# Optimization experiments

Measured on AMD Instinct MI355X. Metric: run time of the kernel, lower is better.

## Reference

```python
import jax, jax.numpy as jnp
import numpy as np

N_NODES = 50000


def setup_inputs() -> dict:
    key = jax.random.key(0)
    ks = jax.random.split(key, 5)
    d_in, d_out = 512, 512
    n_edges = 800000
    x = jax.random.normal(ks[0], (N_NODES, d_in), dtype=jnp.float32)
    edge_index = jax.random.randint(ks[1], (2, n_edges), 0, N_NODES, dtype=jnp.int64)
    s = 1.0 / np.sqrt(d_in)
    W_l = jax.random.uniform(ks[2], (d_out, d_in), dtype=jnp.float32, minval=-s, maxval=s)
    b_l = jax.random.uniform(ks[3], (d_out,), dtype=jnp.float32, minval=-s, maxval=s)
    W_r = jax.random.uniform(ks[4], (d_out, d_in), dtype=jnp.float32, minval=-s, maxval=s)
    return {"x": x, "edge_index": edge_index, "W_l": W_l, "b_l": b_l, "W_r": W_r}


def reference(x, edge_index, W_l, b_l, W_r):
    # lin_l: dense transform before aggregation
    x_l = x @ W_l.T + b_l                       # [N, d_out]
    src, dst = edge_index[0], edge_index[1]
    # sparse adjacency matmul (SAGE mean-neighbor aggregation):
    # out_l[i] = mean_{j in N(i)} x_l[j]
    agg = jax.ops.segment_sum(x_l[src], dst, num_segments=N_NODES)   # [N, d_out]
    deg = jax.ops.segment_sum(jnp.ones_like(src, dtype=x.dtype), dst,
                              num_segments=N_NODES)                  # [N]
    out_l = agg / jnp.maximum(deg, 1.0)[:, None]
    # lin_r: self-loop transform (no bias)
    out_r = x @ W_r.T
    return out_l + out_r
```

## Files before the change

kernel.cpp:

```cpp
#include <hip/hip_runtime.h>

typedef __bf16 bf16x8 __attribute__((ext_vector_type(8)));
typedef float floatx4 __attribute__((ext_vector_type(4)));
typedef float floatx2 __attribute__((ext_vector_type(2)));
typedef unsigned short ushortx8 __attribute__((ext_vector_type(8)));

__device__ __forceinline__ unsigned short f2b(float f) {
    union { float f; unsigned u; } v; v.f = f;
    unsigned r = v.u + 0x7fffu + ((v.u >> 16) & 1u);
    return (unsigned short)(r >> 16);
}


__global__ void scan_kernel(const int* __restrict__ deg, int* __restrict__ off,
                            int n, int nE) {
    __shared__ int s[256];
    __shared__ int base_s;
    int b = blockIdx.x, t = threadIdx.x;
    int lim = b * 1024;
    int acc = 0;
    for (int i = t * 4; i < lim; i += 1024) {
        int4 v = *(const int4*)(deg + i);
        acc += v.x + v.y + v.z + v.w;
    }
    s[t] = acc; __syncthreads();
    for (int o = 128; o > 0; o >>= 1) { if (t < o) s[t] += s[t + o]; __syncthreads(); }
    if (t == 0) base_s = s[0];
    __syncthreads();
    int idx = b * 1024 + t * 4;
    int a0 = (idx     < n) ? deg[idx]     : 0;
    int a1 = (idx + 1 < n) ? deg[idx + 1] : 0;
    int a2 = (idx + 2 < n) ? deg[idx + 2] : 0;
    int a3 = (idx + 3 < n) ? deg[idx + 3] : 0;
    int tsum = a0 + a1 + a2 + a3;
    s[t] = tsum; __syncthreads();
    for (int o = 1; o < 256; o <<= 1) {
        int u = (t >= o) ? s[t - o] : 0;
        __syncthreads();
        s[t] += u;
        __syncthreads();
    }
    int excl = s[t] - tsum + base_s;
    if (idx     < n) off[idx]     = excl;
    if (idx + 1 < n) off[idx + 1] = excl + a0;
    if (idx + 2 < n) off[idx + 2] = excl + a0 + a1;
    if (idx + 3 < n) off[idx + 3] = excl + a0 + a1 + a2;
    if (b == 0 && t == 0) off[n] = nE;
}

__global__ void fill_kernel(const int* __restrict__ src, const int* __restrict__ dst,
                            const int* __restrict__ off, int* __restrict__ cursor,
                            int* __restrict__ csr, int nE) {
    int e = blockIdx.x * blockDim.x + threadIdx.x;
    if (e < nE) {
        int d = dst[e];
        int pos = atomicAdd(&cursor[d], 1);
        csr[off[d] + pos] = src[e];
    }
}


__global__ void conv_kernel(const float* __restrict__ x, unsigned short* __restrict__ Abuf,
                            unsigned char* __restrict__ X8,
                            const float* __restrict__ Wl, const float* __restrict__ Wr,
                            unsigned short* __restrict__ Wcat,
                            const int* __restrict__ dst, int* __restrict__ deg, int nE,
                            int Mreal, long nx) {
    long t = (long)blockIdx.x * blockDim.x + threadIdx.x;
    if (t < nx) {
        long row = t >> 6;
        int c8 = (int)(t & 63) * 8;
        if (row < Mreal) {
            const float4* p4 = (const float4*)(x + row * 512 + c8);
            float4 v0 = p4[0], v1 = p4[1];
            ushortx8 o8;
            o8[0] = f2b(v0.x); o8[1] = f2b(v0.y); o8[2] = f2b(v0.z); o8[3] = f2b(v0.w);
            o8[4] = f2b(v1.x); o8[5] = f2b(v1.y); o8[6] = f2b(v1.z); o8[7] = f2b(v1.w);
            *(ushortx8*)(Abuf + row * 1024 + 512 + c8) = o8;
            unsigned int pa = __builtin_amdgcn_cvt_pk_fp8_f32(v0.x, v0.y, 0, false);
            pa = __builtin_amdgcn_cvt_pk_fp8_f32(v0.z, v0.w, pa, true);
            unsigned int pb = __builtin_amdgcn_cvt_pk_fp8_f32(v1.x, v1.y, 0, false);
            pb = __builtin_amdgcn_cvt_pk_fp8_f32(v1.z, v1.w, pb, true);
            *(uint2*)(X8 + row * 512 + c8) = make_uint2(pa, pb);
        } else {
            ushortx8 z = {0, 0, 0, 0, 0, 0, 0, 0};
            *(ushortx8*)(Abuf + row * 1024 + c8) = z;
            *(ushortx8*)(Abuf + row * 1024 + 512 + c8) = z;
        }
    } else {
        long u = t - nx;
        if (u < 65536) {
            int o = (int)(u >> 7);
            int c8 = (int)(u & 127) * 8;
            const float* p = (c8 < 512) ? (Wl + o * 512 + c8) : (Wr + o * 512 + (c8 - 512));
            float4 v0 = ((const float4*)p)[0], v1 = ((const float4*)p)[1];
            ushortx8 o8;
            o8[0] = f2b(v0.x); o8[1] = f2b(v0.y); o8[2] = f2b(v0.z); o8[3] = f2b(v0.w);
            o8[4] = f2b(v1.x); o8[5] = f2b(v1.y); o8[6] = f2b(v1.z); o8[7] = f2b(v1.w);
            *(ushortx8*)(Wcat + (long)o * 1024 + c8) = o8;
        } else {
            long v = u - 65536;
            if (v < nE) atomicAdd(&deg[dst[v]], 1);
        }
    }
}


__device__ __forceinline__ uint2 ldrow(const unsigned char* __restrict__ X8, int myi, int idx, int l) {
    int s = __builtin_amdgcn_readlane(myi, idx);
    return *(const uint2*)(X8 + (long)s * 512 + l * 8);
}

__device__ __forceinline__ void accum(float* a, uint2 p) {
    floatx2 f0 = __builtin_amdgcn_cvt_pk_f32_fp8(p.x, false);
    floatx2 f1 = __builtin_amdgcn_cvt_pk_f32_fp8(p.x, true);
    floatx2 f2 = __builtin_amdgcn_cvt_pk_f32_fp8(p.y, false);
    floatx2 f3 = __builtin_amdgcn_cvt_pk_f32_fp8(p.y, true);
    a[0] += f0[0]; a[1] += f0[1]; a[2] += f1[0]; a[3] += f1[1];
    a[4] += f2[0]; a[5] += f2[1]; a[6] += f3[0]; a[7] += f3[1];
}

__global__ void agg_kernel(const unsigned char* __restrict__ X8,
                           const int* __restrict__ off, const int* __restrict__ csr,
                           unsigned short* __restrict__ Abuf_w, int n) {
    int wid = (int)((blockIdx.x * (long)blockDim.x + threadIdx.x) >> 6);
    int l = threadIdx.x & 63;
    if (wid >= n) return;
    int beg = off[wid], end = off[wid + 1];
    float a[8] = {};
    int e = beg;
    while (e < end) {
        int cnt = end - e; if (cnt > 64) cnt = 64;
        int myi = csr[e + (l < cnt ? l : cnt - 1)];
        int c1 = cnt - 1;
        uint2 b0 = ldrow(X8, myi, 0, l);
        uint2 b1 = ldrow(X8, myi, 1 < c1 ? 1 : c1, l);
        uint2 b2 = ldrow(X8, myi, 2 < c1 ? 2 : c1, l);
        uint2 b3 = ldrow(X8, myi, 3 < c1 ? 3 : c1, l);
        int j = 0;
        for (; j + 4 < cnt; j += 4) {
            uint2 n0 = ldrow(X8, myi, j + 4, l);
            uint2 n1 = ldrow(X8, myi, j + 5 < c1 ? j + 5 : c1, l);
            uint2 n2 = ldrow(X8, myi, j + 6 < c1 ? j + 6 : c1, l);
            uint2 n3 = ldrow(X8, myi, j + 7 < c1 ? j + 7 : c1, l);
            accum(a, b0); accum(a, b1); accum(a, b2); accum(a, b3);
            b0 = n0; b1 = n1; b2 = n2; b3 = n3;
        }
        int rem = cnt - j;
        accum(a, b0);
        if (rem > 1) accum(a, b1);
        if (rem > 2) accum(a, b2);
        if (rem > 3) accum(a, b3);
        e += cnt;
    }
    int d = end - beg;
    float inv = 1.0f / (float)(d > 0 ? d : 1);
    ushortx8 o8;
#pragma unroll
    for (int i = 0; i < 8; i++) o8[i] = f2b(a[i] * inv);
    *(ushortx8*)(Abuf_w + (long)wid * 1024 + l * 8) = o8;
}


__global__ __launch_bounds__(256, 3)
void gemm_kernel(const unsigned short* __restrict__ A, const unsigned short* __restrict__ B,
                 const float* __restrict__ bl, const int* __restrict__ deg,
                 float* __restrict__ out, int Mreal, int nby) {
    int L = blockIdx.x;
    int by = (L >> 5) * 8 + (L & 7);
    int bx = (L >> 3) & 3;
    if (by >= nby) return;

    __shared__ unsigned short As[3 * 128 * 32];
    __shared__ unsigned short Bs[3 * 128 * 32];
    int tid = threadIdx.x;
    int w = tid >> 6, l = tid & 63;
    long i0 = (long)by * 128;
    int n0 = bx * 128;
    int wm = (w >> 1) * 64, wn = (w & 1) * 64;
    int r = l & 15, q = l >> 4;
    int srow = l >> 2;
    int cg8 = ((l & 3) ^ ((srow >> 1) & 3)) * 8;
    int p8 = (q ^ ((r >> 1) & 3)) * 8;

    floatx4 acc[4][4] = {};

    auto stage = [&](int buf, int k0) {
#pragma unroll
        for (int j = 0; j < 2; j++) {
            int s = w * 2 + j;
            int row = s * 16 + srow;
            const unsigned short* ga = A + (i0 + row) * 1024 + k0 + cg8;
            const unsigned short* gb = B + (long)(n0 + row) * 1024 + k0 + cg8;
            __builtin_amdgcn_global_load_lds(
                (__attribute__((address_space(1))) void*)(uintptr_t)ga,
                (__attribute__((address_space(3))) void*)(uintptr_t)(As + buf * 4096 + s * 512), 16, 0, 0);
            __builtin_amdgcn_global_load_lds(
                (__attribute__((address_space(1))) void*)(uintptr_t)gb,
                (__attribute__((address_space(3))) void*)(uintptr_t)(Bs + buf * 4096 + s * 512), 16, 0, 0);
        }
    };

    auto compute = [&](int cur) {
        bf16x8 af[4], bfr[4];
        const unsigned short* Ab = As + cur * 4096;
        const unsigned short* Bb = Bs + cur * 4096;
#pragma unroll
        for (int a = 0; a < 4; a++)
            af[a] = *(const bf16x8*)(Ab + (wm + a * 16 + r) * 32 + p8);
#pragma unroll
        for (int b = 0; b < 4; b++)
            bfr[b] = *(const bf16x8*)(Bb + (wn + b * 16 + r) * 32 + p8);
        __builtin_amdgcn_s_setprio(1);
#pragma unroll
        for (int a = 0; a < 4; a++)
#pragma unroll
            for (int b = 0; b < 4; b++)
                acc[a][b] = __builtin_amdgcn_mfma_f32_16x16x32_bf16(bfr[b], af[a], acc[a][b], 0, 0, 0);
        __builtin_amdgcn_s_setprio(0);
    };

    stage(0, 0);
    stage(1, 32);
    int cur = 0;
    for (int t = 0; t < 31; ++t) {
        asm volatile("s_waitcnt vmcnt(4)" ::: "memory");
        __builtin_amdgcn_sched_barrier(0);
        __builtin_amdgcn_s_barrier();
        __builtin_amdgcn_sched_barrier(0);
        if (t + 2 < 32) {
            int nb2 = cur + 2; if (nb2 >= 3) nb2 -= 3;
            stage(nb2, (t + 2) * 32);
        }
        compute(cur);
        cur++; if (cur >= 3) cur -= 3;
    }
    asm volatile("s_waitcnt vmcnt(0)" ::: "memory");
    __builtin_amdgcn_sched_barrier(0);
    __builtin_amdgcn_s_barrier();
    __builtin_amdgcn_sched_barrier(0);
    compute(cur);

#pragma unroll
    for (int a = 0; a < 4; a++) {
        long row = i0 + wm + a * 16 + r;
        if (row < Mreal) {
            bool hasdeg = deg[row] > 0;
#pragma unroll
            for (int b = 0; b < 4; b++) {
                int col0 = n0 + wn + b * 16 + q * 4;
                floatx4 v = acc[a][b];
                if (hasdeg) {
                    float4 bb = *(const float4*)(bl + col0);
                    v[0] += bb.x; v[1] += bb.y; v[2] += bb.z; v[3] += bb.w;
                }
                *(floatx4*)(out + row * 512 + col0) = v;
            }
        }
    }
}


extern "C" void kernel_launch(void* const* d_in, const int* in_sizes, int n_in,
                              void* d_out, int out_size, void* d_ws, size_t ws_size,
                              hipStream_t stream) {
    const float* x  = (const float*)d_in[0];
    const int* eidx = (const int*)d_in[1];
    const float* Wl = (const float*)d_in[2];
    const float* bl = (const float*)d_in[3];
    const float* Wr = (const float*)d_in[4];
    float* out = (float*)d_out;

    int N  = in_sizes[0] / 512;
    int nE = in_sizes[1] / 2;
    const int* src = eidx;
    const int* dst = eidx + nE;
    int Mpad = (N + 127) & ~127;
    int nb = (N + 1023) / 1024;
    int nby = Mpad / 128;

    char* w = (char*)d_ws;
    size_t o = 0;
    auto alloc = [&](size_t bytes) { void* p = w + o; o = (o + bytes + 255) & ~255UL; return p; };
    int* deg    = (int*)alloc((size_t)N * 4);
    int* cursor = (int*)alloc((size_t)N * 4);
    int* off    = (int*)alloc((size_t)(N + 1) * 4);
    int* csr    = (int*)alloc((size_t)nE * 4);
    unsigned short* Wcat = (unsigned short*)alloc((size_t)512 * 1024 * 2);
    unsigned short* Abuf = (unsigned short*)alloc((size_t)Mpad * 1024 * 2);
    unsigned char*  X8   = (unsigned char*)alloc((size_t)Mpad * 512);
    if (o > ws_size) return;

    hipMemsetAsync(deg, 0, (size_t)((char*)cursor - (char*)deg) + (size_t)N * 4, stream);

    long nx = (long)Mpad * 64;
    long ntot = nx + 65536 + nE;
    conv_kernel<<<(int)((ntot + 255) / 256), 256, 0, stream>>>(x, Abuf, X8, Wl, Wr, Wcat,
                                                               dst, deg, nE, N, nx);
    scan_kernel<<<nb, 256, 0, stream>>>(deg, off, N, nE);
    fill_kernel<<<(nE + 255) / 256, 256, 0, stream>>>(src, dst, off, cursor, csr, nE);
    agg_kernel<<<(N * 64 + 255) / 256, 256, 0, stream>>>(X8, off, csr, Abuf, N);

    int nbyp = (nby + 7) & ~7;
    gemm_kernel<<<nbyp * 4, 256, 0, stream>>>(Abuf, Wcat, bl, deg, out, N, nby);
}
```

Measured before the change: 395.7 us.

## Merge conversion, scan, CSR fill and aggregation into one cooperative kernel

Replaces four separate launches (conversion/degree count, prefix scan, CSR fill, mean aggregation) with one persistent cooperative kernel of 768 blocks that uses grid-stride loops and grid.sync between phases. The aim is to remove per-launch overhead and the idle tails between dependent kernels. In exchange, every phase runs on a fixed grid, so the scan phase needs nb <= 768 and the bandwidth-heavy phases may see less latency hiding than the oversubscribed launches had. Grid-wide barriers also add their own cost.

```diff
diff --git a/kernel.cpp b/kernel.cpp
--- a/kernel.cpp
+++ b/kernel.cpp
@@ -1,4 +1,7 @@
 #include <hip/hip_runtime.h>
+#include <hip/hip_cooperative_groups.h>
+
+namespace cg = cooperative_groups;
 
 typedef __bf16 bf16x8 __attribute__((ext_vector_type(8)));
 typedef float floatx4 __attribute__((ext_vector_type(4)));
@@ -10,101 +13,6 @@
     unsigned r = v.u + 0x7fffu + ((v.u >> 16) & 1u);
     return (unsigned short)(r >> 16);
 }
-
-
-__global__ void scan_kernel(const int* __restrict__ deg, int* __restrict__ off,
-                            int n, int nE) {
-    __shared__ int s[256];
-    __shared__ int base_s;
-    int b = blockIdx.x, t = threadIdx.x;
-    int lim = b * 1024;
-    int acc = 0;
-    for (int i = t * 4; i < lim; i += 1024) {
-        int4 v = *(const int4*)(deg + i);
-        acc += v.x + v.y + v.z + v.w;
-    }
-    s[t] = acc; __syncthreads();
-    for (int o = 128; o > 0; o >>= 1) { if (t < o) s[t] += s[t + o]; __syncthreads(); }
-    if (t == 0) base_s = s[0];
-    __syncthreads();
-    int idx = b * 1024 + t * 4;
-    int a0 = (idx     < n) ? deg[idx]     : 0;
-    int a1 = (idx + 1 < n) ? deg[idx + 1] : 0;
-    int a2 = (idx + 2 < n) ? deg[idx + 2] : 0;
-    int a3 = (idx + 3 < n) ? deg[idx + 3] : 0;
-    int tsum = a0 + a1 + a2 + a3;
-    s[t] = tsum; __syncthreads();
-    for (int o = 1; o < 256; o <<= 1) {
-        int u = (t >= o) ? s[t - o] : 0;
-        __syncthreads();
-        s[t] += u;
-        __syncthreads();
-    }
-    int excl = s[t] - tsum + base_s;
-    if (idx     < n) off[idx]     = excl;
-    if (idx + 1 < n) off[idx + 1] = excl + a0;
-    if (idx + 2 < n) off[idx + 2] = excl + a0 + a1;
-    if (idx + 3 < n) off[idx + 3] = excl + a0 + a1 + a2;
-    if (b == 0 && t == 0) off[n] = nE;
-}
-
-__global__ void fill_kernel(const int* __restrict__ src, const int* __restrict__ dst,
-                            const int* __restrict__ off, int* __restrict__ cursor,
-                            int* __restrict__ csr, int nE) {
-    int e = blockIdx.x * blockDim.x + threadIdx.x;
-    if (e < nE) {
-        int d = dst[e];
-        int pos = atomicAdd(&cursor[d], 1);
-        csr[off[d] + pos] = src[e];
-    }
-}
-
-
-__global__ void conv_kernel(const float* __restrict__ x, unsigned short* __restrict__ Abuf,
-                            unsigned char* __restrict__ X8,
-                            const float* __restrict__ Wl, const float* __restrict__ Wr,
-                            unsigned short* __restrict__ Wcat,
-                            const int* __restrict__ dst, int* __restrict__ deg, int nE,
-                            int Mreal, long nx) {
-    long t = (long)blockIdx.x * blockDim.x + threadIdx.x;
-    if (t < nx) {
-        long row = t >> 6;
-        int c8 = (int)(t & 63) * 8;
-        if (row < Mreal) {
-            const float4* p4 = (const float4*)(x + row * 512 + c8);
-            float4 v0 = p4[0], v1 = p4[1];
-            ushortx8 o8;
-            o8[0] = f2b(v0.x); o8[1] = f2b(v0.y); o8[2] = f2b(v0.z); o8[3] = f2b(v0.w);
-            o8[4] = f2b(v1.x); o8[5] = f2b(v1.y); o8[6] = f2b(v1.z); o8[7] = f2b(v1.w);
-            *(ushortx8*)(Abuf + row * 1024 + 512 + c8) = o8;
-            unsigned int pa = __builtin_amdgcn_cvt_pk_fp8_f32(v0.x, v0.y, 0, false);
-            pa = __builtin_amdgcn_cvt_pk_fp8_f32(v0.z, v0.w, pa, true);
-            unsigned int pb = __builtin_amdgcn_cvt_pk_fp8_f32(v1.x, v1.y, 0, false);
-            pb = __builtin_amdgcn_cvt_pk_fp8_f32(v1.z, v1.w, pb, true);
-            *(uint2*)(X8 + row * 512 + c8) = make_uint2(pa, pb);
-        } else {
-            ushortx8 z = {0, 0, 0, 0, 0, 0, 0, 0};
-            *(ushortx8*)(Abuf + row * 1024 + c8) = z;
-            *(ushortx8*)(Abuf + row * 1024 + 512 + c8) = z;
-        }
-    } else {
-        long u = t - nx;
-        if (u < 65536) {
-            int o = (int)(u >> 7);
-            int c8 = (int)(u & 127) * 8;
-            const float* p = (c8 < 512) ? (Wl + o * 512 + c8) : (Wr + o * 512 + (c8 - 512));
-            float4 v0 = ((const float4*)p)[0], v1 = ((const float4*)p)[1];
-            ushortx8 o8;
-            o8[0] = f2b(v0.x); o8[1] = f2b(v0.y); o8[2] = f2b(v0.z); o8[3] = f2b(v0.w);
-            o8[4] = f2b(v1.x); o8[5] = f2b(v1.y); o8[6] = f2b(v1.z); o8[7] = f2b(v1.w);
-            *(ushortx8*)(Wcat + (long)o * 1024 + c8) = o8;
-        } else {
-            long v = u - 65536;
-            if (v < nE) atomicAdd(&deg[dst[v]], 1);
-        }
-    }
-}
-
 
 __device__ __forceinline__ uint2 ldrow(const unsigned char* __restrict__ X8, int myi, int idx, int l) {
     int s = __builtin_amdgcn_readlane(myi, idx);
@@ -120,45 +28,150 @@
     a[4] += f2[0]; a[5] += f2[1]; a[6] += f3[0]; a[7] += f3[1];
 }
 
-__global__ void agg_kernel(const unsigned char* __restrict__ X8,
-                           const int* __restrict__ off, const int* __restrict__ csr,
-                           unsigned short* __restrict__ Abuf_w, int n) {
-    int wid = (int)((blockIdx.x * (long)blockDim.x + threadIdx.x) >> 6);
-    int l = threadIdx.x & 63;
-    if (wid >= n) return;
-    int beg = off[wid], end = off[wid + 1];
-    float a[8] = {};
-    int e = beg;
-    while (e < end) {
-        int cnt = end - e; if (cnt > 64) cnt = 64;
-        int myi = csr[e + (l < cnt ? l : cnt - 1)];
-        int c1 = cnt - 1;
-        uint2 b0 = ldrow(X8, myi, 0, l);
-        uint2 b1 = ldrow(X8, myi, 1 < c1 ? 1 : c1, l);
-        uint2 b2 = ldrow(X8, myi, 2 < c1 ? 2 : c1, l);
-        uint2 b3 = ldrow(X8, myi, 3 < c1 ? 3 : c1, l);
-        int j = 0;
-        for (; j + 4 < cnt; j += 4) {
-            uint2 n0 = ldrow(X8, myi, j + 4, l);
-            uint2 n1 = ldrow(X8, myi, j + 5 < c1 ? j + 5 : c1, l);
-            uint2 n2 = ldrow(X8, myi, j + 6 < c1 ? j + 6 : c1, l);
-            uint2 n3 = ldrow(X8, myi, j + 7 < c1 ? j + 7 : c1, l);
-            accum(a, b0); accum(a, b1); accum(a, b2); accum(a, b3);
-            b0 = n0; b1 = n1; b2 = n2; b3 = n3;
-        }
-        int rem = cnt - j;
-        accum(a, b0);
-        if (rem > 1) accum(a, b1);
-        if (rem > 2) accum(a, b2);
-        if (rem > 3) accum(a, b3);
-        e += cnt;
-    }
-    int d = end - beg;
-    float inv = 1.0f / (float)(d > 0 ? d : 1);
-    ushortx8 o8;
-#pragma unroll
-    for (int i = 0; i < 8; i++) o8[i] = f2b(a[i] * inv);
-    *(ushortx8*)(Abuf_w + (long)wid * 1024 + l * 8) = o8;
+
+__global__ __launch_bounds__(256, 3)
+void mega_kernel(const float* __restrict__ x, unsigned short* __restrict__ Abuf,
+                 unsigned char* __restrict__ X8,
+                 const float* __restrict__ Wl, const float* __restrict__ Wr,
+                 unsigned short* __restrict__ Wcat,
+                 const int* __restrict__ src, const int* __restrict__ dst,
+                 int* __restrict__ deg, int* __restrict__ cursor,
+                 int* __restrict__ off, int* __restrict__ csr,
+                 int N, int nE, int nb, long nx) {
+    cg::grid_group grid = cg::this_grid();
+    const long gsz = (long)gridDim.x * blockDim.x;
+    const long gtid = (long)blockIdx.x * blockDim.x + threadIdx.x;
+
+    {
+        const long ntot = nx + 65536 + nE;
+        for (long t = gtid; t < ntot; t += gsz) {
+            if (t < nx) {
+                long row = t >> 6;
+                int c8 = (int)(t & 63) * 8;
+                if (row < N) {
+                    const float4* p4 = (const float4*)(x + row * 512 + c8);
+                    float4 v0 = p4[0], v1 = p4[1];
+                    ushortx8 o8;
+                    o8[0] = f2b(v0.x); o8[1] = f2b(v0.y); o8[2] = f2b(v0.z); o8[3] = f2b(v0.w);
+                    o8[4] = f2b(v1.x); o8[5] = f2b(v1.y); o8[6] = f2b(v1.z); o8[7] = f2b(v1.w);
+                    *(ushortx8*)(Abuf + row * 1024 + 512 + c8) = o8;
+                    unsigned int pa = __builtin_amdgcn_cvt_pk_fp8_f32(v0.x, v0.y, 0, false);
+                    pa = __builtin_amdgcn_cvt_pk_fp8_f32(v0.z, v0.w, pa, true);
+                    unsigned int pb = __builtin_amdgcn_cvt_pk_fp8_f32(v1.x, v1.y, 0, false);
+                    pb = __builtin_amdgcn_cvt_pk_fp8_f32(v1.z, v1.w, pb, true);
+                    *(uint2*)(X8 + row * 512 + c8) = make_uint2(pa, pb);
+                } else {
+                    ushortx8 z = {0, 0, 0, 0, 0, 0, 0, 0};
+                    *(ushortx8*)(Abuf + row * 1024 + c8) = z;
+                    *(ushortx8*)(Abuf + row * 1024 + 512 + c8) = z;
+                }
+            } else {
+                long u = t - nx;
+                if (u < 65536) {
+                    int o = (int)(u >> 7);
+                    int c8 = (int)(u & 127) * 8;
+                    const float* p = (c8 < 512) ? (Wl + o * 512 + c8) : (Wr + o * 512 + (c8 - 512));
+                    float4 v0 = ((const float4*)p)[0], v1 = ((const float4*)p)[1];
+                    ushortx8 o8;
+                    o8[0] = f2b(v0.x); o8[1] = f2b(v0.y); o8[2] = f2b(v0.z); o8[3] = f2b(v0.w);
+                    o8[4] = f2b(v1.x); o8[5] = f2b(v1.y); o8[6] = f2b(v1.z); o8[7] = f2b(v1.w);
+                    *(ushortx8*)(Wcat + (long)o * 1024 + c8) = o8;
+                } else {
+                    long v = u - 65536;
+                    if (v < nE) atomicAdd(&deg[dst[v]], 1);
+                }
+            }
+        }
+    }
+    __threadfence();
+    grid.sync();
+
+    {
+        __shared__ int s[256];
+        __shared__ int base_s;
+        int b = blockIdx.x, t = threadIdx.x;
+        if (b < nb) {
+            int lim = b * 1024;
+            int a = 0;
+            for (int i = t * 4; i < lim; i += 1024) {
+                int4 v = *(const int4*)(deg + i);
+                a += v.x + v.y + v.z + v.w;
+            }
+            s[t] = a; __syncthreads();
+            for (int o = 128; o > 0; o >>= 1) { if (t < o) s[t] += s[t + o]; __syncthreads(); }
+            if (t == 0) base_s = s[0];
+            __syncthreads();
+            int idx = b * 1024 + t * 4;
+            int a0 = (idx     < N) ? deg[idx]     : 0;
+            int a1 = (idx + 1 < N) ? deg[idx + 1] : 0;
+            int a2 = (idx + 2 < N) ? deg[idx + 2] : 0;
+            int a3 = (idx + 3 < N) ? deg[idx + 3] : 0;
+            int tsum = a0 + a1 + a2 + a3;
+            s[t] = tsum; __syncthreads();
+            for (int o = 1; o < 256; o <<= 1) {
+                int u = (t >= o) ? s[t - o] : 0;
+                __syncthreads();
+                s[t] += u;
+                __syncthreads();
+            }
+            int excl = s[t] - tsum + base_s;
+            if (idx     < N) off[idx]     = excl;
+            if (idx + 1 < N) off[idx + 1] = excl + a0;
+            if (idx + 2 < N) off[idx + 2] = excl + a0 + a1;
+            if (idx + 3 < N) off[idx + 3] = excl + a0 + a1 + a2;
+            if (b == 0 && t == 0) off[N] = nE;
+        }
+    }
+    __threadfence();
+    grid.sync();
+
+    for (long e = gtid; e < nE; e += gsz) {
+        int d = dst[e];
+        int pos = atomicAdd(&cursor[d], 1);
+        csr[off[d] + pos] = src[e];
+    }
+    __threadfence();
+    grid.sync();
+
+    {
+        const int nwaves = (int)(gsz >> 6);
+        const int l = threadIdx.x & 63;
+        for (int wid = (int)(gtid >> 6); wid < N; wid += nwaves) {
+            int beg = off[wid], end = off[wid + 1];
+            float a[8] = {};
+            int e = beg;
+            while (e < end) {
+                int cnt = end - e; if (cnt > 64) cnt = 64;
+                int myi = csr[e + (l < cnt ? l : cnt - 1)];
+                int c1 = cnt - 1;
+                uint2 b0 = ldrow(X8, myi, 0, l);
+                uint2 b1 = ldrow(X8, myi, 1 < c1 ? 1 : c1, l);
+                uint2 b2 = ldrow(X8, myi, 2 < c1 ? 2 : c1, l);
+                uint2 b3 = ldrow(X8, myi, 3 < c1 ? 3 : c1, l);
+                int j = 0;
+                for (; j + 4 < cnt; j += 4) {
+                    uint2 n0 = ldrow(X8, myi, j + 4, l);
+                    uint2 n1 = ldrow(X8, myi, j + 5 < c1 ? j + 5 : c1, l);
+                    uint2 n2 = ldrow(X8, myi, j + 6 < c1 ? j + 6 : c1, l);
+                    uint2 n3 = ldrow(X8, myi, j + 7 < c1 ? j + 7 : c1, l);
+                    accum(a, b0); accum(a, b1); accum(a, b2); accum(a, b3);
+                    b0 = n0; b1 = n1; b2 = n2; b3 = n3;
+                }
+                int rem = cnt - j;
+                accum(a, b0);
+                if (rem > 1) accum(a, b1);
+                if (rem > 2) accum(a, b2);
+                if (rem > 3) accum(a, b3);
+                e += cnt;
+            }
+            int d = end - beg;
+            float inv = 1.0f / (float)(d > 0 ? d : 1);
+            ushortx8 o8;
+#pragma unroll
+            for (int i = 0; i < 8; i++) o8[i] = f2b(a[i] * inv);
+            *(ushortx8*)(Abuf + (long)wid * 1024 + l * 8) = o8;
+        }
+    }
 }
 
 
@@ -294,12 +307,14 @@
     hipMemsetAsync(deg, 0, (size_t)((char*)cursor - (char*)deg) + (size_t)N * 4, stream);
 
     long nx = (long)Mpad * 64;
-    long ntot = nx + 65536 + nE;
-    conv_kernel<<<(int)((ntot + 255) / 256), 256, 0, stream>>>(x, Abuf, X8, Wl, Wr, Wcat,
-                                                               dst, deg, nE, N, nx);
-    scan_kernel<<<nb, 256, 0, stream>>>(deg, off, N, nE);
-    fill_kernel<<<(nE + 255) / 256, 256, 0, stream>>>(src, dst, off, cursor, csr, nE);
-    agg_kernel<<<(N * 64 + 255) / 256, 256, 0, stream>>>(X8, off, csr, Abuf, N);
+
+    void* margs[] = {
+        (void*)&x, (void*)&Abuf, (void*)&X8, (void*)&Wl, (void*)&Wr, (void*)&Wcat,
+        (void*)&src, (void*)&dst, (void*)&deg, (void*)&cursor, (void*)&off, (void*)&csr,
+        (void*)&N, (void*)&nE, (void*)&nb, (void*)&nx
+    };
+    hipLaunchCooperativeKernel((const void*)mega_kernel, dim3(768), dim3(256),
+                               margs, 0, stream);
 
     int nbyp = (nby + 7) & ~7;
     gemm_kernel<<<nbyp * 4, 256, 0, stream>>>(Abuf, Wcat, bl, deg, out, N, nby);
```

Result: slower. 819.3 us (+107.0%).

## Gather two neighbor rows per wave with 16-byte loads; split GEMM into four launches

Applied to the files above, without the earlier changes.

The aggregation kernel now has each half-wave load a different neighbor row using 16-byte loads, so each wave handles two edges per step. The two halves' partial sums are combined with a cross-half shuffle before the bf16 store. An odd trailing edge is handled by the lower half only. Separately, the GEMM is launched as four sequential grids over row-block ranges via a new by0 offset, which adds launch overhead and changes block scheduling.

```diff
diff --git a/kernel.cpp b/kernel.cpp
--- a/kernel.cpp
+++ b/kernel.cpp
@@ -106,18 +106,24 @@
 }
 
 
-__device__ __forceinline__ uint2 ldrow(const unsigned char* __restrict__ X8, int myi, int idx, int l) {
-    int s = __builtin_amdgcn_readlane(myi, idx);
-    return *(const uint2*)(X8 + (long)s * 512 + l * 8);
-}
-
-__device__ __forceinline__ void accum(float* a, uint2 p) {
-    floatx2 f0 = __builtin_amdgcn_cvt_pk_f32_fp8(p.x, false);
-    floatx2 f1 = __builtin_amdgcn_cvt_pk_f32_fp8(p.x, true);
-    floatx2 f2 = __builtin_amdgcn_cvt_pk_f32_fp8(p.y, false);
-    floatx2 f3 = __builtin_amdgcn_cvt_pk_f32_fp8(p.y, true);
-    a[0] += f0[0]; a[1] += f0[1]; a[2] += f1[0]; a[3] += f1[1];
-    a[4] += f2[0]; a[5] += f2[1]; a[6] += f3[0]; a[7] += f3[1];
+__device__ __forceinline__ void accum16(float* a, uint4 p) {
+    floatx2 f;
+    f = __builtin_amdgcn_cvt_pk_f32_fp8(p.x, false); a[0]  += f[0]; a[1]  += f[1];
+    f = __builtin_amdgcn_cvt_pk_f32_fp8(p.x, true);  a[2]  += f[0]; a[3]  += f[1];
+    f = __builtin_amdgcn_cvt_pk_f32_fp8(p.y, false); a[4]  += f[0]; a[5]  += f[1];
+    f = __builtin_amdgcn_cvt_pk_f32_fp8(p.y, true);  a[6]  += f[0]; a[7]  += f[1];
+    f = __builtin_amdgcn_cvt_pk_f32_fp8(p.z, false); a[8]  += f[0]; a[9]  += f[1];
+    f = __builtin_amdgcn_cvt_pk_f32_fp8(p.z, true);  a[10] += f[0]; a[11] += f[1];
+    f = __builtin_amdgcn_cvt_pk_f32_fp8(p.w, false); a[12] += f[0]; a[13] += f[1];
+    f = __builtin_amdgcn_cvt_pk_f32_fp8(p.w, true);  a[14] += f[0]; a[15] += f[1];
+}
+
+__device__ __forceinline__ uint4 ldpair(const unsigned char* __restrict__ X8, int myi,
+                                        int p, int h, int m) {
+    int s0 = __builtin_amdgcn_readlane(myi, 2 * p);
+    int s1 = __builtin_amdgcn_readlane(myi, 2 * p + 1);
+    long s = h ? s1 : s0;
+    return *(const uint4*)(X8 + s * 512 + m * 16);
 }
 
 __global__ void agg_kernel(const unsigned char* __restrict__ X8,
@@ -125,49 +131,62 @@
                            unsigned short* __restrict__ Abuf_w, int n) {
     int wid = (int)((blockIdx.x * (long)blockDim.x + threadIdx.x) >> 6);
     int l = threadIdx.x & 63;
+    int h = l >> 5, m = l & 31;
     if (wid >= n) return;
     int beg = off[wid], end = off[wid + 1];
-    float a[8] = {};
+    float a[16] = {};
     int e = beg;
     while (e < end) {
         int cnt = end - e; if (cnt > 64) cnt = 64;
         int myi = csr[e + (l < cnt ? l : cnt - 1)];
-        int c1 = cnt - 1;
-        uint2 b0 = ldrow(X8, myi, 0, l);
-        uint2 b1 = ldrow(X8, myi, 1 < c1 ? 1 : c1, l);
-        uint2 b2 = ldrow(X8, myi, 2 < c1 ? 2 : c1, l);
-        uint2 b3 = ldrow(X8, myi, 3 < c1 ? 3 : c1, l);
-        int j = 0;
-        for (; j + 4 < cnt; j += 4) {
-            uint2 n0 = ldrow(X8, myi, j + 4, l);
-            uint2 n1 = ldrow(X8, myi, j + 5 < c1 ? j + 5 : c1, l);
-            uint2 n2 = ldrow(X8, myi, j + 6 < c1 ? j + 6 : c1, l);
-            uint2 n3 = ldrow(X8, myi, j + 7 < c1 ? j + 7 : c1, l);
-            accum(a, b0); accum(a, b1); accum(a, b2); accum(a, b3);
-            b0 = n0; b1 = n1; b2 = n2; b3 = n3;
-        }
-        int rem = cnt - j;
-        accum(a, b0);
-        if (rem > 1) accum(a, b1);
-        if (rem > 2) accum(a, b2);
-        if (rem > 3) accum(a, b3);
+        int np = cnt >> 1;
+        if (np > 0) {
+            int c1 = np - 1;
+            uint4 b0 = ldpair(X8, myi, 0, h, m);
+            uint4 b1 = ldpair(X8, myi, 1 < c1 ? 1 : c1, h, m);
+            uint4 b2 = ldpair(X8, myi, 2 < c1 ? 2 : c1, h, m);
+            uint4 b3 = ldpair(X8, myi, 3 < c1 ? 3 : c1, h, m);
+            int j = 0;
+            for (; j + 4 < np; j += 4) {
+                uint4 n0 = ldpair(X8, myi, j + 4, h, m);
+                uint4 n1 = ldpair(X8, myi, j + 5 < c1 ? j + 5 : c1, h, m);
+                uint4 n2 = ldpair(X8, myi, j + 6 < c1 ? j + 6 : c1, h, m);
+                uint4 n3 = ldpair(X8, myi, j + 7 < c1 ? j + 7 : c1, h, m);
+                accum16(a, b0); accum16(a, b1); accum16(a, b2); accum16(a, b3);
+                b0 = n0; b1 = n1; b2 = n2; b3 = n3;
+            }
+            int rem = np - j;
+            accum16(a, b0);
+            if (rem > 1) accum16(a, b1);
+            if (rem > 2) accum16(a, b2);
+            if (rem > 3) accum16(a, b3);
+        }
+        if (cnt & 1) {
+            int s = __builtin_amdgcn_readlane(myi, cnt - 1);
+            if (h == 0) {
+                uint4 v = *(const uint4*)(X8 + (long)s * 512 + m * 16);
+                accum16(a, v);
+            }
+        }
         e += cnt;
     }
+#pragma unroll
+    for (int i = 0; i < 16; i++) a[i] += __shfl_xor(a[i], 32, 64);
     int d = end - beg;
     float inv = 1.0f / (float)(d > 0 ? d : 1);
     ushortx8 o8;
 #pragma unroll
-    for (int i = 0; i < 8; i++) o8[i] = f2b(a[i] * inv);
-    *(ushortx8*)(Abuf_w + (long)wid * 1024 + l * 8) = o8;
+    for (int i = 0; i < 8; i++) o8[i] = f2b(a[h * 8 + i] * inv);
+    *(ushortx8*)(Abuf_w + (long)wid * 1024 + m * 16 + h * 8) = o8;
 }
 
 
 __global__ __launch_bounds__(256, 3)
 void gemm_kernel(const unsigned short* __restrict__ A, const unsigned short* __restrict__ B,
                  const float* __restrict__ bl, const int* __restrict__ deg,
-                 float* __restrict__ out, int Mreal, int nby) {
+                 float* __restrict__ out, int Mreal, int nby, int by0) {
     int L = blockIdx.x;
-    int by = (L >> 5) * 8 + (L & 7);
+    int by = by0 + (L >> 5) * 8 + (L & 7);
     int bx = (L >> 3) & 3;
     if (by >= nby) return;
 
@@ -301,6 +320,10 @@
     fill_kernel<<<(nE + 255) / 256, 256, 0, stream>>>(src, dst, off, cursor, csr, nE);
     agg_kernel<<<(N * 64 + 255) / 256, 256, 0, stream>>>(X8, off, csr, Abuf, N);
 
-    int nbyp = (nby + 7) & ~7;
-    gemm_kernel<<<nbyp * 4, 256, 0, stream>>>(Abuf, Wcat, bl, deg, out, N, nby);
-}
+    int qs = (((nby + 3) >> 2) + 7) & ~7;
+    for (int qq = 0; qq < 4; ++qq) {
+        int by0 = qq * qs;
+        if (by0 < nby)
+            gemm_kernel<<<qs * 4, 256, 0, stream>>>(Abuf, Wcat, bl, deg, out, N, nby, by0);
+    }
+}
```

New measurement: 420.9 us. 1.06x slower.

## Gather four neighbor rows per wave with 32-byte loads in aggregation

Applied to the files above, without the earlier changes.

The aggregation kernel now splits each wave into four 16-lane groups. Each group loads a different neighbor's FP8 row using two 16-byte loads per lane instead of one 8-byte load, and the partial sums are reduced across groups with xor shuffles at the end. The conversion kernel also processes 16 elements per thread with wider stores. This aims to cut the number of memory instructions and the serial per-neighbor iterations, at the cost of 32 accumulator registers per lane, extra shuffles, and a remainder path for degrees not divisible by four.

```diff
diff --git a/kernel.cpp b/kernel.cpp
--- a/kernel.cpp
+++ b/kernel.cpp
@@ -65,30 +65,39 @@
                             const float* __restrict__ Wl, const float* __restrict__ Wr,
                             unsigned short* __restrict__ Wcat,
                             const int* __restrict__ dst, int* __restrict__ deg, int nE,
-                            int Mreal, long nx) {
+                            int Mreal, long nx2) {
     long t = (long)blockIdx.x * blockDim.x + threadIdx.x;
-    if (t < nx) {
-        long row = t >> 6;
-        int c8 = (int)(t & 63) * 8;
+    if (t < nx2) {
+        long row = t >> 5;
+        int c16 = (int)(t & 31) * 16;
         if (row < Mreal) {
-            const float4* p4 = (const float4*)(x + row * 512 + c8);
-            float4 v0 = p4[0], v1 = p4[1];
-            ushortx8 o8;
-            o8[0] = f2b(v0.x); o8[1] = f2b(v0.y); o8[2] = f2b(v0.z); o8[3] = f2b(v0.w);
-            o8[4] = f2b(v1.x); o8[5] = f2b(v1.y); o8[6] = f2b(v1.z); o8[7] = f2b(v1.w);
-            *(ushortx8*)(Abuf + row * 1024 + 512 + c8) = o8;
+            const float4* p4 = (const float4*)(x + row * 512 + c16);
+            float4 v0 = p4[0], v1 = p4[1], v2 = p4[2], v3 = p4[3];
+            ushortx8 oA, oB;
+            oA[0] = f2b(v0.x); oA[1] = f2b(v0.y); oA[2] = f2b(v0.z); oA[3] = f2b(v0.w);
+            oA[4] = f2b(v1.x); oA[5] = f2b(v1.y); oA[6] = f2b(v1.z); oA[7] = f2b(v1.w);
+            oB[0] = f2b(v2.x); oB[1] = f2b(v2.y); oB[2] = f2b(v2.z); oB[3] = f2b(v2.w);
+            oB[4] = f2b(v3.x); oB[5] = f2b(v3.y); oB[6] = f2b(v3.z); oB[7] = f2b(v3.w);
+            *(ushortx8*)(Abuf + row * 1024 + 512 + c16)     = oA;
+            *(ushortx8*)(Abuf + row * 1024 + 512 + c16 + 8) = oB;
             unsigned int pa = __builtin_amdgcn_cvt_pk_fp8_f32(v0.x, v0.y, 0, false);
             pa = __builtin_amdgcn_cvt_pk_fp8_f32(v0.z, v0.w, pa, true);
             unsigned int pb = __builtin_amdgcn_cvt_pk_fp8_f32(v1.x, v1.y, 0, false);
             pb = __builtin_amdgcn_cvt_pk_fp8_f32(v1.z, v1.w, pb, true);
-            *(uint2*)(X8 + row * 512 + c8) = make_uint2(pa, pb);
+            unsigned int pc = __builtin_amdgcn_cvt_pk_fp8_f32(v2.x, v2.y, 0, false);
+            pc = __builtin_amdgcn_cvt_pk_fp8_f32(v2.z, v2.w, pc, true);
+            unsigned int pd = __builtin_amdgcn_cvt_pk_fp8_f32(v3.x, v3.y, 0, false);
+            pd = __builtin_amdgcn_cvt_pk_fp8_f32(v3.z, v3.w, pd, true);
+            *(uint4*)(X8 + row * 512 + c16) = make_uint4(pa, pb, pc, pd);
         } else {
             ushortx8 z = {0, 0, 0, 0, 0, 0, 0, 0};
-            *(ushortx8*)(Abuf + row * 1024 + c8) = z;
-            *(ushortx8*)(Abuf + row * 1024 + 512 + c8) = z;
+            *(ushortx8*)(Abuf + row * 1024 + c16)           = z;
+            *(ushortx8*)(Abuf + row * 1024 + c16 + 8)       = z;
+            *(ushortx8*)(Abuf + row * 1024 + 512 + c16)     = z;
+            *(ushortx8*)(Abuf + row * 1024 + 512 + c16 + 8) = z;
         }
     } else {
-        long u = t - nx;
+        long u = t - nx2;
         if (u < 65536) {
             int o = (int)(u >> 7);
             int c8 = (int)(u & 127) * 8;
@@ -106,18 +115,27 @@
 }
 
 
-__device__ __forceinline__ uint2 ldrow(const unsigned char* __restrict__ X8, int myi, int idx, int l) {
-    int s = __builtin_amdgcn_readlane(myi, idx);
-    return *(const uint2*)(X8 + (long)s * 512 + l * 8);
-}
-
-__device__ __forceinline__ void accum(float* a, uint2 p) {
-    floatx2 f0 = __builtin_amdgcn_cvt_pk_f32_fp8(p.x, false);
-    floatx2 f1 = __builtin_amdgcn_cvt_pk_f32_fp8(p.x, true);
-    floatx2 f2 = __builtin_amdgcn_cvt_pk_f32_fp8(p.y, false);
-    floatx2 f3 = __builtin_amdgcn_cvt_pk_f32_fp8(p.y, true);
-    a[0] += f0[0]; a[1] += f0[1]; a[2] += f1[0]; a[3] += f1[1];
-    a[4] += f2[0]; a[5] += f2[1]; a[6] += f3[0]; a[7] += f3[1];
+struct U8v { uint4 lo; uint4 hi; };
+
+__device__ __forceinline__ U8v ldquad(const unsigned char* __restrict__ X8, int myi,
+                                      int p, int qh, int m) {
+    int s0 = __builtin_amdgcn_readlane(myi, 4 * p);
+    int s1 = __builtin_amdgcn_readlane(myi, 4 * p + 1);
+    int s2 = __builtin_amdgcn_readlane(myi, 4 * p + 2);
+    int s3 = __builtin_amdgcn_readlane(myi, 4 * p + 3);
+    int s = (qh == 0) ? s0 : (qh == 1) ? s1 : (qh == 2) ? s2 : s3;
+    const uint4* q = (const uint4*)(X8 + (long)s * 512 + m * 32);
+    U8v r; r.lo = q[0]; r.hi = q[1]; return r;
+}
+
+__device__ __forceinline__ void accum32(float* a, const U8v& p) {
+    floatx2 f;
+#define ACC4(d, base) \
+    f = __builtin_amdgcn_cvt_pk_f32_fp8(d, false); a[base] += f[0]; a[base + 1] += f[1]; \
+    f = __builtin_amdgcn_cvt_pk_f32_fp8(d, true);  a[base + 2] += f[0]; a[base + 3] += f[1];
+    ACC4(p.lo.x, 0)  ACC4(p.lo.y, 4)  ACC4(p.lo.z, 8)  ACC4(p.lo.w, 12)
+    ACC4(p.hi.x, 16) ACC4(p.hi.y, 20) ACC4(p.hi.z, 24) ACC4(p.hi.w, 28)
+#undef ACC4
 }
 
 __global__ void agg_kernel(const unsigned char* __restrict__ X8,
@@ -125,40 +143,62 @@
                            unsigned short* __restrict__ Abuf_w, int n) {
     int wid = (int)((blockIdx.x * (long)blockDim.x + threadIdx.x) >> 6);
     int l = threadIdx.x & 63;
+    int qh = l >> 4, m = l & 15;
     if (wid >= n) return;
     int beg = off[wid], end = off[wid + 1];
-    float a[8] = {};
+    float a[32] = {};
     int e = beg;
     while (e < end) {
         int cnt = end - e; if (cnt > 64) cnt = 64;
         int myi = csr[e + (l < cnt ? l : cnt - 1)];
-        int c1 = cnt - 1;
-        uint2 b0 = ldrow(X8, myi, 0, l);
-        uint2 b1 = ldrow(X8, myi, 1 < c1 ? 1 : c1, l);
-        uint2 b2 = ldrow(X8, myi, 2 < c1 ? 2 : c1, l);
-        uint2 b3 = ldrow(X8, myi, 3 < c1 ? 3 : c1, l);
-        int j = 0;
-        for (; j + 4 < cnt; j += 4) {
-            uint2 n0 = ldrow(X8, myi, j + 4, l);
-            uint2 n1 = ldrow(X8, myi, j + 5 < c1 ? j + 5 : c1, l);
-            uint2 n2 = ldrow(X8, myi, j + 6 < c1 ? j + 6 : c1, l);
-            uint2 n3 = ldrow(X8, myi, j + 7 < c1 ? j + 7 : c1, l);
-            accum(a, b0); accum(a, b1); accum(a, b2); accum(a, b3);
-            b0 = n0; b1 = n1; b2 = n2; b3 = n3;
-        }
-        int rem = cnt - j;
-        accum(a, b0);
-        if (rem > 1) accum(a, b1);
-        if (rem > 2) accum(a, b2);
-        if (rem > 3) accum(a, b3);
+        int np = cnt >> 2;
+        int rem = cnt & 3;
+        if (np > 0) {
+            int c1 = np - 1;
+            U8v b0 = ldquad(X8, myi, 0, qh, m);
+            U8v b1 = ldquad(X8, myi, 1 < c1 ? 1 : c1, qh, m);
+            U8v b2 = ldquad(X8, myi, 2 < c1 ? 2 : c1, qh, m);
+            U8v b3 = ldquad(X8, myi, 3 < c1 ? 3 : c1, qh, m);
+            int j = 0;
+            for (; j + 4 < np; j += 4) {
+                U8v n0 = ldquad(X8, myi, j + 4, qh, m);
+                U8v n1 = ldquad(X8, myi, j + 5 < c1 ? j + 5 : c1, qh, m);
+                U8v n2 = ldquad(X8, myi, j + 6 < c1 ? j + 6 : c1, qh, m);
+                U8v n3 = ldquad(X8, myi, j + 7 < c1 ? j + 7 : c1, qh, m);
+                accum32(a, b0); accum32(a, b1); accum32(a, b2); accum32(a, b3);
+                b0 = n0; b1 = n1; b2 = n2; b3 = n3;
+            }
+            int r2 = np - j;
+            accum32(a, b0);
+            if (r2 > 1) accum32(a, b1);
+            if (r2 > 2) accum32(a, b2);
+            if (r2 > 3) accum32(a, b3);
+        }
+        if (rem) {
+            int i0 = np << 2;
+            int i1 = (i0 + 1 < cnt) ? i0 + 1 : cnt - 1;
+            int i2 = (i0 + 2 < cnt) ? i0 + 2 : cnt - 1;
+            int s0 = __builtin_amdgcn_readlane(myi, i0);
+            int s1 = __builtin_amdgcn_readlane(myi, i1);
+            int s2 = __builtin_amdgcn_readlane(myi, i2);
+            int s = (qh == 1) ? s1 : (qh == 2) ? s2 : s0;
+            const uint4* q = (const uint4*)(X8 + (long)s * 512 + m * 32);
+            uint4 lo = q[0], hi = q[1];
+            if (qh < rem) { U8v tv; tv.lo = lo; tv.hi = hi; accum32(a, tv); }
+        }
         e += cnt;
+    }
+#pragma unroll
+    for (int i = 0; i < 32; i++) {
+        a[i] += __shfl_xor(a[i], 16, 64);
+        a[i] += __shfl_xor(a[i], 32, 64);
     }
     int d = end - beg;
     float inv = 1.0f / (float)(d > 0 ? d : 1);
     ushortx8 o8;
 #pragma unroll
-    for (int i = 0; i < 8; i++) o8[i] = f2b(a[i] * inv);
-    *(ushortx8*)(Abuf_w + (long)wid * 1024 + l * 8) = o8;
+    for (int i = 0; i < 8; i++) o8[i] = f2b(a[qh * 8 + i] * inv);
+    *(ushortx8*)(Abuf_w + (long)wid * 1024 + m * 32 + qh * 8) = o8;
 }
 
 
@@ -293,10 +333,10 @@
 
     hipMemsetAsync(deg, 0, (size_t)((char*)cursor - (char*)deg) + (size_t)N * 4, stream);
 
-    long nx = (long)Mpad * 64;
-    long ntot = nx + 65536 + nE;
+    long nx2 = (long)Mpad * 32;
+    long ntot = nx2 + 65536 + nE;
     conv_kernel<<<(int)((ntot + 255) / 256), 256, 0, stream>>>(x, Abuf, X8, Wl, Wr, Wcat,
-                                                               dst, deg, nE, N, nx);
+                                                               dst, deg, nE, N, nx2);
     scan_kernel<<<nb, 256, 0, stream>>>(deg, off, N, nE);
     fill_kernel<<<(nE + 255) / 256, 256, 0, stream>>>(src, dst, off, cursor, csr, nE);
     agg_kernel<<<(N * 64 + 255) / 256, 256, 0, stream>>>(X8, off, csr, Abuf, N);
```

After: 496.2 us. 1.25x slower.
